# Optimization experiments

Hardware: AMD Instinct MI355X
Metric: run time of the kernel (lower is better)

The kernel has to match this reference:

```python
import jax, jax.numpy as jnp
import numpy as np

N = 8_388_608        # cohort size (2^23)
T_MAX = 1_000_000    # distinct time values -> ~8 ties per unique time


def setup_inputs() -> dict:
    key = jax.random.key(0)
    k1, k2, k3 = jax.random.split(key, 3)
    x = jax.random.normal(k1, (N,), dtype=jnp.float32)  # risk scores
    times = jax.random.randint(k2, (N,), 0, T_MAX).astype(jnp.float32)
    events = (jax.random.uniform(k3, (N,)) < 0.7).astype(jnp.float32)
    target = jnp.stack([times, events], axis=1)  # [N, 2] = [time, event]
    return {"input": x, "target": target}


def _cox_breslow_sqrt_loss(x, target):
    times = target[:, 0]
    events_all = target[:, 1]
    n = x.shape[0]
    # Sort by descending time (risk set = prefix in this ordering).
    sort_idx = jnp.argsort(-times)
    t = times[sort_idx]
    ev = events_all[sort_idx]
    xs = x[sort_idx]
    # Stable prefix log-sum-exp over the risk set.
    log_cum = jax.lax.cumlogsumexp(xs)
    # end_idx[i] = last index of the tie group containing i (groups are
    # contiguous after sorting). Reverse running-min over positions of
    # group-last elements.
    is_last = jnp.concatenate([t[:-1] != t[1:], jnp.ones((1,), dtype=bool)])
    pos = jnp.where(is_last, jnp.arange(n), n)
    end_idx = jnp.flip(jax.lax.cummin(jnp.flip(pos)))
    # Breslow: -sum(x*ev) + sum_groups logcum[group_end] * (#events in group)
    #        == -sum((x - logcum[end_idx]) * ev)
    loss = -jnp.sum((xs - log_cum[end_idx]) * ev)
    # reduction='mean' -> sqrt(loss / n)
    return jnp.sqrt(loss / n)


def reference(input, target):
    return _cox_breslow_sqrt_loss(input, target)
```

## Files before the change

kernel.cpp:

```cpp
#include <hip/hip_runtime.h>
#include <math.h>

#define TMAX 1000000
#define BINW 4096
#define BINSHIFT 12
#define NBIN 245
#define PADN (NBIN * BINW)
#define TILE 8192
#define NTHR 512
#define CAP 36864
#define CURSOR_STRIDE 16
#define BT_STRIDE 8
#define FIXSCALE 65536.0f
#define INV_FIXSCALE (1.0 / 65536.0)

#define OFF_SCAL     0
#define OFF_DONE     16
#define OFF_CURSOR   64
#define OFF_BINTOT   15744
#define OFF_PAYLOAD  31488
#define MEMSET_BYTES 31424
#define NEED_FULL    ((size_t)OFF_PAYLOAD + (size_t)NBIN * CAP * 4)
#define FB_BINTOT    15744
#define FB_CEXCL     17792
#define FB_BEXP      31488
#define FB_BEV       (FB_BEXP + PADN * 4)
#define NEED_MIN     ((size_t)FB_BEV + PADN * 4)

__device__ __forceinline__ int clamp_tau(float t) {
    int tau = (int)t;
    if (tau < 0) tau = 0;
    if (tau >= TMAX) tau = TMAX - 1;
    return tau;
}

__device__ __forceinline__ unsigned enc_payload(float xv, float tv, float ev_f, int* bin_out) {
    int tau = clamp_tau(tv);
    *bin_out = tau >> BINSHIFT;
    int fine = tau & (BINW - 1);
    float ex = __expf(xv);
    unsigned bb = __float_as_uint(ex);
    bb = (bb + 0x7FFFu + ((bb >> 16) & 1u)) >> 16;
    unsigned ev = (ev_f != 0.0f) ? 1u : 0u;
    return (bb << 16) | ((unsigned)fine << 1) | ev;
}

__device__ __forceinline__ float dec_exp(unsigned p) {
    return __uint_as_float((p >> 16) << 16);
}

__device__ __forceinline__ void hist1(unsigned long long* hist, unsigned p) {
    float ex = dec_exp(p);
    unsigned fx = __float2uint_rn(ex * FIXSCALE);
    unsigned long long add = ((unsigned long long)(p & 1u) << 48) | (unsigned long long)fx;
    atomicAdd(&hist[(p >> 1) & (BINW - 1)], add);
}

__device__ __forceinline__ void hist4(unsigned long long* hist, uint4 pv) {
    hist1(hist, pv.x); hist1(hist, pv.y); hist1(hist, pv.z); hist1(hist, pv.w);
}

__global__ __launch_bounds__(NTHR) void k_scatter(const float* __restrict__ x,
                                                  const float* __restrict__ tgt,
                                                  unsigned* __restrict__ cursor,
                                                  unsigned* __restrict__ payload,
                                                  double* __restrict__ bintot,
                                                  double* __restrict__ evx_out, int n) {
    __shared__ unsigned cnt[256];
    __shared__ unsigned lpre[256];
    __shared__ unsigned pay_lds[TILE];
    __shared__ unsigned char binof2[TILE / 2];
    __shared__ unsigned wtot_s[8];
    __shared__ double wpart[8];
    const int t = threadIdx.x;
    const int lane = t & 63;
    const int wv = t >> 6;
    if (t < 256) cnt[t] = 0;
    __syncthreads();

    const int tile0 = blockIdx.x * TILE;
    const int tilecount = min(TILE, n - tile0);
    unsigned pay[16], meta[16];
    double evx = 0.0;

    if (tilecount == TILE) {
        const float4* x4 = (const float4*)x;
        const float4* t4 = (const float4*)tgt;
        const int g0 = blockIdx.x * (TILE / 4);
#pragma unroll
        for (int j = 0; j < 4; ++j) {
            const int g = g0 + j * NTHR + t;
            float4 xv = x4[g];
            float4 ta = t4[2 * g];
            float4 tb = t4[2 * g + 1];
            float xs[4] = {xv.x, xv.y, xv.z, xv.w};
            float ts[4] = {ta.x, ta.z, tb.x, tb.z};
            float es[4] = {ta.y, ta.w, tb.y, tb.w};
#pragma unroll
            for (int e = 0; e < 4; ++e) {
                int bin;
                unsigned p = enc_payload(xs[e], ts[e], es[e], &bin);
                unsigned r = atomicAdd(&cnt[bin], 1u);
                pay[4 * j + e] = p;
                meta[4 * j + e] = ((unsigned)bin << 13) | r;
                if (p & 1) evx += (double)xs[e];
            }
        }
    } else {
        const float2* tg2 = (const float2*)tgt;
#pragma unroll
        for (int j = 0; j < 16; ++j) {
            int idx = tile0 + j * NTHR + t;
            if (idx < n) {
                float xv = x[idx];
                float2 te = tg2[idx];
                int bin;
                unsigned p = enc_payload(xv, te.x, te.y, &bin);
                unsigned r = atomicAdd(&cnt[bin], 1u);
                pay[j] = p;
                meta[j] = ((unsigned)bin << 13) | r;
                if (p & 1) evx += (double)xv;
            } else {
                meta[j] = 0xFFFFFFFFu;
            }
        }
    }
    __syncthreads();

    const unsigned c = (t < 256) ? cnt[t] : 0u;
    unsigned pfx = c;
#pragma unroll
    for (int d = 1; d < 64; d <<= 1) {
        unsigned u = __shfl_up(pfx, d);
        if (lane >= d) pfx += u;
    }
    if (lane == 63) wtot_s[wv] = pfx;
    __syncthreads();
    unsigned wbase = 0;
    if (t < 256) {
        for (int w = 0; w < wv; ++w) wbase += wtot_s[w];
    }
    const unsigned excl = (t < 256) ? (wbase + pfx - c) : 0u;
    if (t < 256) lpre[t] = excl;

    if (t < NBIN && c) cnt[t] = atomicAdd(&cursor[t * CURSOR_STRIDE], c);

    if (t < NBIN && c) {
        for (unsigned j = (excl + 1) >> 1; 2 * j < excl + c; ++j)
            binof2[j] = (unsigned char)t;
    }
    __syncthreads();

#pragma unroll
    for (int j = 0; j < 16; ++j) {
        if (meta[j] != 0xFFFFFFFFu) {
            unsigned bin = meta[j] >> 13;
            pay_lds[lpre[bin] + (meta[j] & 0x1FFFu)] = pay[j];
        }
    }
    __syncthreads();

    if (t < NBIN && c) {
        float s = 0.0f;
        for (unsigned k = excl; k < excl + c; ++k) s += dec_exp(pay_lds[k]);
        unsafeAtomicAdd(&bintot[t * BT_STRIDE], (double)s);
    }

    for (int k = t; k < tilecount; k += NTHR) {
        unsigned b = binof2[(unsigned)k >> 1];
        if (t & 1) {
            while ((unsigned)k >= lpre[b + 1]) ++b;
        }
        unsigned pos = cnt[b] + ((unsigned)k - lpre[b]);
        if (pos < CAP) payload[(size_t)b * CAP + pos] = pay_lds[k];
    }

#pragma unroll
    for (int d = 32; d > 0; d >>= 1) {
        double u = __shfl_down(evx, d);
        if (lane + d < 64) evx += u;
    }
    if (lane == 0) wpart[wv] = evx;
    __syncthreads();
    if (t == 0) {
        double s = 0.0;
        for (int w = 0; w < 8; ++w) s += wpart[w];
        atomicAdd(evx_out, s);
    }
}

__global__ __launch_bounds__(1024) void k_fused(const unsigned* __restrict__ payload,
                                                const unsigned* __restrict__ cursor,
                                                const double* __restrict__ bintot,
                                                double* __restrict__ scal,
                                                unsigned* __restrict__ done,
                                                float* __restrict__ out, int n) {
    __shared__ unsigned long long hist[BINW];
    __shared__ double wsumA[16];
    __shared__ double wsum[16];
    __shared__ double bcast;
    const int b = blockIdx.x;
    const int t = threadIdx.x;
    const int lane = t & 63;
    const int wv = t >> 6;

#pragma unroll
    for (int j = 0; j < BINW / 1024; ++j) hist[t + j * 1024] = 0ull;
    __syncthreads();

    unsigned cnt = cursor[b * CURSOR_STRIDE];
    if (cnt > CAP) cnt = CAP;
    const unsigned* seg = payload + (size_t)b * CAP;
    const uint4* seg4 = (const uint4*)seg;
    const unsigned n4 = cnt >> 2;
    unsigned i = t;
    for (; i + 1024 < n4; i += 2048) {
        uint4 a = seg4[i];
        uint4 c4 = seg4[i + 1024];
        hist4(hist, a);
        hist4(hist, c4);
    }
    for (; i < n4; i += 1024) hist4(hist, seg4[i]);
    for (unsigned k = (n4 << 2) + t; k < cnt; k += 1024) hist1(hist, seg[k]);
    __syncthreads();

    double ce = 0.0;
    for (int idx = b + 1 + t; idx < NBIN; idx += 1024) ce += bintot[idx * BT_STRIDE];
#pragma unroll
    for (int d = 32; d > 0; d >>= 1) {
        double u = __shfl_down(ce, d);
        if (lane + d < 64) ce += u;
    }
    if (lane == 0) wsumA[wv] = ce;
    __syncthreads();
    if (t == 0) {
        double s = 0.0;
        for (int w = 0; w < 16; ++w) s += wsumA[w];
        bcast = s;
    }
    __syncthreads();
    const double cexcl = bcast;

    const int tb = t * 4;
    double vex[4];
    unsigned vcnt[4];
    double segtot = 0.0;
#pragma unroll
    for (int j = 0; j < 4; ++j) {
        unsigned long long h = hist[tb + j];
        vex[j] = (double)(h & 0xFFFFFFFFFFFFull) * INV_FIXSCALE;
        vcnt[j] = (unsigned)(h >> 48);
        segtot += vex[j];
    }
    double isuf = segtot;
#pragma unroll
    for (int d = 1; d < 64; d <<= 1) {
        double u = __shfl_down(isuf, d);
        if (lane + d < 64) isuf += u;
    }
    if (lane == 0) wsum[wv] = isuf;
    __syncthreads();
    double wexcl = 0.0;
    for (int w = wv + 1; w < 16; ++w) wexcl += wsum[w];

    double run = cexcl + wexcl + (isuf - segtot);
    double local = 0.0;
#pragma unroll
    for (int j = 3; j >= 0; --j) {
        run += vex[j];
        if (vcnt[j]) local += (double)vcnt[j] * log(run);
    }

#pragma unroll
    for (int d = 32; d > 0; d >>= 1) {
        double u = __shfl_down(local, d);
        if (lane + d < 64) local += u;
    }
    if (lane == 0) wsumA[wv] = local;
    __syncthreads();
    if (t == 0) {
        double s = 0.0;
        for (int w = 0; w < 16; ++w) s += wsumA[w];
        unsafeAtomicAdd(&scal[1], s);
        __threadfence();
        unsigned tk = atomicAdd(done, 1u);
        if (tk == NBIN - 1) {
            double ld = unsafeAtomicAdd(&scal[1], 0.0);
            double loss = ld - scal[0];
            if (loss < 0.0) loss = 0.0;
            out[0] = (float)sqrt(loss / (double)n);
        }
    }
}

__global__ void k_accum(const float* __restrict__ x, const float* __restrict__ tgt,
                        float* __restrict__ bexp, float* __restrict__ bev,
                        double* __restrict__ evx_out, int ngroups) {
    double local = 0.0;
    const int nt = gridDim.x * blockDim.x;
    const int tid = blockIdx.x * blockDim.x + threadIdx.x;
    const float4* x4 = (const float4*)x;
    const float4* t4 = (const float4*)tgt;
    for (int g = tid; g < ngroups; g += nt) {
        float4 xv = x4[g];
        float4 ta = t4[2 * g];
        float4 tb = t4[2 * g + 1];
        float xs[4] = {xv.x, xv.y, xv.z, xv.w};
        float ts[4] = {ta.x, ta.z, tb.x, tb.z};
        float es[4] = {ta.y, ta.w, tb.y, tb.w};
#pragma unroll
        for (int j = 0; j < 4; ++j) {
            int tau = clamp_tau(ts[j]);
            unsafeAtomicAdd(&bexp[tau], __expf(xs[j]));
            if (es[j] != 0.0f) unsafeAtomicAdd(&bev[tau], es[j]);
            local += (double)(es[j] * xs[j]);
        }
    }
    __shared__ double sm[256];
    sm[threadIdx.x] = local;
    __syncthreads();
    for (int s = 128; s > 0; s >>= 1) {
        if (threadIdx.x < s) sm[threadIdx.x] += sm[threadIdx.x + s];
        __syncthreads();
    }
    if (threadIdx.x == 0) atomicAdd(evx_out, sm[0]);
}

__global__ void k_chunksum(const float* __restrict__ bexp, double* __restrict__ bintot) {
    const int b = blockIdx.x;
    double local = 0.0;
    for (int i = b * BINW + (int)threadIdx.x; i < (b + 1) * BINW; i += (int)blockDim.x)
        local += (double)bexp[i];
    __shared__ double sm[256];
    sm[threadIdx.x] = local;
    __syncthreads();
    for (int s = 128; s > 0; s >>= 1) {
        if (threadIdx.x < s) sm[threadIdx.x] += sm[threadIdx.x + s];
        __syncthreads();
    }
    if (threadIdx.x == 0) bintot[b] = sm[0];
}

__global__ __launch_bounds__(256) void k_scanbins(const double* __restrict__ bintot,
                                                  double* __restrict__ cexcl) {
    __shared__ double sm[256];
    const int t = threadIdx.x;
    sm[t] = (t < NBIN) ? bintot[t] : 0.0;
    __syncthreads();
    for (int d = 1; d < 256; d <<= 1) {
        double v = (t + d < 256) ? sm[t + d] : 0.0;
        __syncthreads();
        sm[t] += v;
        __syncthreads();
    }
    double e = (t + 1 < 256) ? sm[t + 1] : 0.0;
    __syncthreads();
    cexcl[t] = e;
}

__global__ __launch_bounds__(256) void k_logdot_g(const float* __restrict__ bexp,
                                                  const float* __restrict__ bev,
                                                  const double* __restrict__ cexcl,
                                                  double* __restrict__ logdot) {
    const int b = blockIdx.x;
    const int t = threadIdx.x;
    const float4* e4 = (const float4*)(bexp + b * BINW + t * 16);
    const float4* v4 = (const float4*)(bev + b * BINW + t * 16);
    float ve[16], vv[16];
#pragma unroll
    for (int q = 0; q < 4; ++q) {
        float4 a = e4[q], bb = v4[q];
        ve[4 * q] = a.x; ve[4 * q + 1] = a.y; ve[4 * q + 2] = a.z; ve[4 * q + 3] = a.w;
        vv[4 * q] = bb.x; vv[4 * q + 1] = bb.y; vv[4 * q + 2] = bb.z; vv[4 * q + 3] = bb.w;
    }
    double segtot = 0.0;
#pragma unroll
    for (int j = 0; j < 16; ++j) segtot += (double)ve[j];
    __shared__ double sm[256];
    sm[t] = segtot;
    __syncthreads();
    for (int d = 1; d < 256; d <<= 1) {
        double v = (t + d < 256) ? sm[t + d] : 0.0;
        __syncthreads();
        sm[t] += v;
        __syncthreads();
    }
    double excl = (t < 255) ? sm[t + 1] : 0.0;
    double run = cexcl[b] + excl;
    double local = 0.0;
#pragma unroll
    for (int j = 15; j >= 0; --j) {
        run += (double)ve[j];
        if (vv[j] > 0.0f) local += (double)vv[j] * log(run);
    }
    __syncthreads();
    sm[t] = local;
    __syncthreads();
    for (int s = 128; s > 0; s >>= 1) {
        if (t < s) sm[t] += sm[t + s];
        __syncthreads();
    }
    if (t == 0) atomicAdd(logdot, sm[0]);
}

__global__ void k_final(const double* __restrict__ scal, float* __restrict__ out, int n) {
    if (threadIdx.x == 0 && blockIdx.x == 0) {
        double loss = scal[1] - scal[0];
        if (loss < 0.0) loss = 0.0;
        out[0] = (float)sqrt(loss / (double)n);
    }
}

extern "C" void kernel_launch(void* const* d_in, const int* in_sizes, int n_in,
                              void* d_out, int out_size, void* d_ws, size_t ws_size,
                              hipStream_t stream) {
    const float* x = (const float*)d_in[0];
    const float* tgt = (const float*)d_in[1];
    float* out = (float*)d_out;
    int n = in_sizes[0];

    char* ws = (char*)d_ws;
    double* scal = (double*)(ws + OFF_SCAL);
    unsigned* done = (unsigned*)(ws + OFF_DONE);
    unsigned* cursor = (unsigned*)(ws + OFF_CURSOR);
    double* bintot = (double*)(ws + OFF_BINTOT);
    unsigned* payload = (unsigned*)(ws + OFF_PAYLOAD);

    if (ws_size >= NEED_FULL) {
        hipMemsetAsync(ws, 0, MEMSET_BYTES, stream);
        const int nblk = (n + TILE - 1) / TILE;
        k_scatter<<<nblk, NTHR, 0, stream>>>(x, tgt, cursor, payload, bintot, scal, n);
        k_fused<<<NBIN, 1024, 0, stream>>>(payload, cursor, bintot, scal, done, out, n);
    } else if (ws_size >= NEED_MIN) {
        float* bexp = (float*)(ws + FB_BEXP);
        float* bev = (float*)(ws + FB_BEV);
        double* bintotF = (double*)(ws + FB_BINTOT);
        double* cexclF = (double*)(ws + FB_CEXCL);
        hipMemsetAsync(ws, 0, NEED_MIN, stream);
        k_accum<<<2048, 256, 0, stream>>>(x, tgt, bexp, bev, scal, n / 4);
        k_chunksum<<<NBIN, 256, 0, stream>>>(bexp, bintotF);
        k_scanbins<<<1, 256, 0, stream>>>(bintotF, cexclF);
        k_logdot_g<<<NBIN, 256, 0, stream>>>(bexp, bev, cexclF, scal + 1);
        k_final<<<1, 1, 0, stream>>>(scal, out, n);
    }
}
```

Measured before the change: 163.3 us.

## Fuse memset, scatter and bin-histogram passes into one cooperative persistent kernel

Replaces the memset, scatter kernel and fused per-bin kernel with a single cooperative kernel that zeroes the workspace, scatters tiles in a grid-stride loop, grid-syncs, then runs the per-bin histogram and log-sum pass. This removes two launch boundaries and the separate memset. In exchange it adds grid-wide barriers and a persistent grid sized from occupancy, capped at 1024 blocks. The per-bin phase now uses 512 threads instead of 1024, and the old path is kept as a fallback if the cooperative launch fails.

```diff
diff --git a/kernel.cpp b/kernel.cpp
--- a/kernel.cpp
+++ b/kernel.cpp
@@ -1,5 +1,8 @@
 #include <hip/hip_runtime.h>
+#include <hip/hip_cooperative_groups.h>
 #include <math.h>
+
+namespace cg = cooperative_groups;
 
 #define TMAX 1000000
 #define BINW 4096
@@ -27,6 +30,8 @@
 #define FB_BEV       (FB_BEXP + PADN * 4)
 #define NEED_MIN     ((size_t)FB_BEV + PADN * 4)
 
+#define SMEM_BYTES 39008
+
 __device__ __forceinline__ int clamp_tau(float t) {
     int tau = (int)t;
     if (tau < 0) tau = 0;
@@ -58,6 +63,254 @@
 
 __device__ __forceinline__ void hist4(unsigned long long* hist, uint4 pv) {
     hist1(hist, pv.x); hist1(hist, pv.y); hist1(hist, pv.z); hist1(hist, pv.w);
+}
+
+__global__ __launch_bounds__(NTHR, 8) void k_all(const float* __restrict__ x,
+                                                 const float* __restrict__ tgt,
+                                                 char* __restrict__ ws,
+                                                 float* __restrict__ out,
+                                                 int n, int ntiles) {
+    __shared__ __align__(16) unsigned char smem[SMEM_BYTES];
+
+    unsigned* cursor = (unsigned*)(ws + OFF_CURSOR);
+    double* bintot = (double*)(ws + OFF_BINTOT);
+    unsigned* payload = (unsigned*)(ws + OFF_PAYLOAD);
+    double* scal = (double*)(ws + OFF_SCAL);
+    unsigned* done = (unsigned*)(ws + OFF_DONE);
+
+    const int t = threadIdx.x;
+    const int lane = t & 63;
+    const int wv = t >> 6;
+
+    cg::grid_group grid = cg::this_grid();
+
+    {
+        unsigned* wsw = (unsigned*)ws;
+        for (unsigned w = blockIdx.x * NTHR + (unsigned)t; w < MEMSET_BYTES / 4;
+             w += gridDim.x * NTHR)
+            wsw[w] = 0u;
+    }
+    __threadfence();
+    grid.sync();
+
+    unsigned* pay_lds = (unsigned*)smem;
+    unsigned char* binof2 = (unsigned char*)(smem + 32768);
+    unsigned* cnt = (unsigned*)(smem + 36864);
+    unsigned* lpre = (unsigned*)(smem + 37888);
+    unsigned* wtot_s = (unsigned*)(smem + 38912);
+    double* wpart = (double*)(smem + 38944);
+
+    double evx = 0.0;
+    for (int tile = blockIdx.x; tile < ntiles; tile += gridDim.x) {
+        __syncthreads();
+        if (t < 256) cnt[t] = 0;
+        __syncthreads();
+
+        const int tile0 = tile * TILE;
+        const int tilecount = min(TILE, n - tile0);
+        unsigned pay[16], meta[16];
+
+        if (tilecount == TILE) {
+            const float4* x4 = (const float4*)x;
+            const float4* t4 = (const float4*)tgt;
+            const int g0 = tile * (TILE / 4);
+#pragma unroll
+            for (int j = 0; j < 4; ++j) {
+                const int g = g0 + j * NTHR + t;
+                float4 xv = x4[g];
+                float4 ta = t4[2 * g];
+                float4 tb = t4[2 * g + 1];
+                float xs[4] = {xv.x, xv.y, xv.z, xv.w};
+                float ts[4] = {ta.x, ta.z, tb.x, tb.z};
+                float es[4] = {ta.y, ta.w, tb.y, tb.w};
+#pragma unroll
+                for (int e = 0; e < 4; ++e) {
+                    int bin;
+                    unsigned p = enc_payload(xs[e], ts[e], es[e], &bin);
+                    unsigned r = atomicAdd(&cnt[bin], 1u);
+                    pay[4 * j + e] = p;
+                    meta[4 * j + e] = ((unsigned)bin << 13) | r;
+                    if (p & 1) evx += (double)xs[e];
+                }
+            }
+        } else {
+            const float2* tg2 = (const float2*)tgt;
+#pragma unroll
+            for (int j = 0; j < 16; ++j) {
+                int idx = tile0 + j * NTHR + t;
+                if (idx < n) {
+                    float xv = x[idx];
+                    float2 te = tg2[idx];
+                    int bin;
+                    unsigned p = enc_payload(xv, te.x, te.y, &bin);
+                    unsigned r = atomicAdd(&cnt[bin], 1u);
+                    pay[j] = p;
+                    meta[j] = ((unsigned)bin << 13) | r;
+                    if (p & 1) evx += (double)xv;
+                } else {
+                    meta[j] = 0xFFFFFFFFu;
+                }
+            }
+        }
+        __syncthreads();
+
+        const unsigned c = (t < 256) ? cnt[t] : 0u;
+        unsigned pfx = c;
+#pragma unroll
+        for (int d = 1; d < 64; d <<= 1) {
+            unsigned u = __shfl_up(pfx, d);
+            if (lane >= d) pfx += u;
+        }
+        if (lane == 63) wtot_s[wv] = pfx;
+        __syncthreads();
+        unsigned wbase = 0;
+        if (t < 256) {
+            for (int w = 0; w < wv; ++w) wbase += wtot_s[w];
+        }
+        const unsigned excl = (t < 256) ? (wbase + pfx - c) : 0u;
+        if (t < 256) lpre[t] = excl;
+
+        if (t < NBIN && c) cnt[t] = atomicAdd(&cursor[t * CURSOR_STRIDE], c);
+
+        if (t < NBIN && c) {
+            for (unsigned j = (excl + 1) >> 1; 2 * j < excl + c; ++j)
+                binof2[j] = (unsigned char)t;
+        }
+        __syncthreads();
+
+#pragma unroll
+        for (int j = 0; j < 16; ++j) {
+            if (meta[j] != 0xFFFFFFFFu) {
+                unsigned bin = meta[j] >> 13;
+                pay_lds[lpre[bin] + (meta[j] & 0x1FFFu)] = pay[j];
+            }
+        }
+        __syncthreads();
+
+        if (t < NBIN && c) {
+            float s = 0.0f;
+            for (unsigned k = excl; k < excl + c; ++k) s += dec_exp(pay_lds[k]);
+            unsafeAtomicAdd(&bintot[t * BT_STRIDE], (double)s);
+        }
+
+        for (int k = t; k < tilecount; k += NTHR) {
+            unsigned b = binof2[(unsigned)k >> 1];
+            if (t & 1) {
+                while ((unsigned)k >= lpre[b + 1]) ++b;
+            }
+            unsigned pos = cnt[b] + ((unsigned)k - lpre[b]);
+            if (pos < CAP) payload[(size_t)b * CAP + pos] = pay_lds[k];
+        }
+    }
+
+#pragma unroll
+    for (int d = 32; d > 0; d >>= 1) {
+        double u = __shfl_down(evx, d);
+        if (lane + d < 64) evx += u;
+    }
+    if (lane == 0) wpart[wv] = evx;
+    __syncthreads();
+    if (t == 0) {
+        double s = 0.0;
+        for (int w = 0; w < 8; ++w) s += wpart[w];
+        atomicAdd(&scal[0], s);
+    }
+
+    __threadfence();
+    grid.sync();
+
+    unsigned long long* hist = (unsigned long long*)smem;
+    double* wsumA = (double*)(smem + 32768);
+    double* wsum = (double*)(smem + 32832);
+    double* bcastp = (double*)(smem + 32896);
+
+    for (int b = blockIdx.x; b < NBIN; b += gridDim.x) {
+        __syncthreads();
+#pragma unroll
+        for (int j = 0; j < BINW / NTHR; ++j) hist[t + j * NTHR] = 0ull;
+        __syncthreads();
+
+        unsigned cntb = cursor[b * CURSOR_STRIDE];
+        if (cntb > CAP) cntb = CAP;
+        const unsigned* seg = payload + (size_t)b * CAP;
+        const uint4* seg4 = (const uint4*)seg;
+        const unsigned n4 = cntb >> 2;
+        unsigned i = t;
+        for (; i + NTHR < n4; i += 2 * NTHR) {
+            uint4 a = seg4[i];
+            uint4 c4 = seg4[i + NTHR];
+            hist4(hist, a);
+            hist4(hist, c4);
+        }
+        for (; i < n4; i += NTHR) hist4(hist, seg4[i]);
+        for (unsigned k = (n4 << 2) + t; k < cntb; k += NTHR) hist1(hist, seg[k]);
+        __syncthreads();
+
+        double ce = 0.0;
+        for (int idx = b + 1 + t; idx < NBIN; idx += NTHR) ce += bintot[idx * BT_STRIDE];
+#pragma unroll
+        for (int d = 32; d > 0; d >>= 1) {
+            double u = __shfl_down(ce, d);
+            if (lane + d < 64) ce += u;
+        }
+        if (lane == 0) wsumA[wv] = ce;
+        __syncthreads();
+        if (t == 0) {
+            double s = 0.0;
+            for (int w = 0; w < 8; ++w) s += wsumA[w];
+            *bcastp = s;
+        }
+        __syncthreads();
+        const double cexcl = *bcastp;
+
+        const int tb = t * (BINW / NTHR);
+        double segtot = 0.0;
+#pragma unroll
+        for (int j = 0; j < BINW / NTHR; ++j)
+            segtot += (double)(hist[tb + j] & 0xFFFFFFFFFFFFull) * INV_FIXSCALE;
+        double isuf = segtot;
+#pragma unroll
+        for (int d = 1; d < 64; d <<= 1) {
+            double u = __shfl_down(isuf, d);
+            if (lane + d < 64) isuf += u;
+        }
+        if (lane == 0) wsum[wv] = isuf;
+        __syncthreads();
+        double wexcl = 0.0;
+        for (int w = wv + 1; w < 8; ++w) wexcl += wsum[w];
+
+        double run = cexcl + wexcl + (isuf - segtot);
+        double local = 0.0;
+#pragma unroll
+        for (int j = BINW / NTHR - 1; j >= 0; --j) {
+            unsigned long long h = hist[tb + j];
+            double v = (double)(h & 0xFFFFFFFFFFFFull) * INV_FIXSCALE;
+            unsigned cc = (unsigned)(h >> 48);
+            run += v;
+            if (cc) local += (double)cc * log(run);
+        }
+
+#pragma unroll
+        for (int d = 32; d > 0; d >>= 1) {
+            double u = __shfl_down(local, d);
+            if (lane + d < 64) local += u;
+        }
+        if (lane == 0) wsumA[wv] = local;
+        __syncthreads();
+        if (t == 0) {
+            double s = 0.0;
+            for (int w = 0; w < 8; ++w) s += wsumA[w];
+            unsafeAtomicAdd(&scal[1], s);
+            __threadfence();
+            unsigned tk = atomicAdd(done, 1u);
+            if (tk == NBIN - 1) {
+                double ld = unsafeAtomicAdd(&scal[1], 0.0);
+                double loss = ld - scal[0];
+                if (loss < 0.0) loss = 0.0;
+                out[0] = (float)sqrt(loss / (double)n);
+            }
+        }
+    }
 }
 
 __global__ __launch_bounds__(NTHR) void k_scatter(const float* __restrict__ x,
@@ -418,20 +671,48 @@
     const float* tgt = (const float*)d_in[1];
     float* out = (float*)d_out;
     int n = in_sizes[0];
-
     char* ws = (char*)d_ws;
-    double* scal = (double*)(ws + OFF_SCAL);
-    unsigned* done = (unsigned*)(ws + OFF_DONE);
-    unsigned* cursor = (unsigned*)(ws + OFF_CURSOR);
-    double* bintot = (double*)(ws + OFF_BINTOT);
-    unsigned* payload = (unsigned*)(ws + OFF_PAYLOAD);
 
     if (ws_size >= NEED_FULL) {
-        hipMemsetAsync(ws, 0, MEMSET_BYTES, stream);
-        const int nblk = (n + TILE - 1) / TILE;
-        k_scatter<<<nblk, NTHR, 0, stream>>>(x, tgt, cursor, payload, bintot, scal, n);
-        k_fused<<<NBIN, 1024, 0, stream>>>(payload, cursor, bintot, scal, done, out, n);
+        static int coop_grid = 0;
+        if (coop_grid == 0) {
+            int dev = 0;
+            (void)hipGetDevice(&dev);
+            int cus = 0;
+            if (hipDeviceGetAttribute(&cus, hipDeviceAttributeMultiprocessorCount, dev) !=
+                    hipSuccess || cus <= 0)
+                cus = 256;
+            int nb = 0;
+            if (hipOccupancyMaxActiveBlocksPerMultiprocessor(&nb, k_all, NTHR, 0) !=
+                    hipSuccess || nb < 1)
+                nb = 1;
+            long g = (long)nb * (long)cus;
+            if (g > 1024) g = 1024;
+            if (g < 1) g = 1;
+            coop_grid = (int)g;
+        }
+        int ntiles = (n + TILE - 1) / TILE;
+        const float* xa = x;
+        const float* ta = tgt;
+        char* wsa = ws;
+        float* oa = out;
+        int na = n, nta = ntiles;
+        void* args[] = {(void*)&xa, (void*)&ta, (void*)&wsa, (void*)&oa, (void*)&na, (void*)&nta};
+        hipError_t err = hipLaunchCooperativeKernel(k_all, dim3(coop_grid), dim3(NTHR),
+                                                    args, 0, stream);
+        if (err != hipSuccess) {
+            double* scal = (double*)(ws + OFF_SCAL);
+            unsigned* done = (unsigned*)(ws + OFF_DONE);
+            unsigned* cursor = (unsigned*)(ws + OFF_CURSOR);
+            double* bintot = (double*)(ws + OFF_BINTOT);
+            unsigned* payload = (unsigned*)(ws + OFF_PAYLOAD);
+            hipMemsetAsync(ws, 0, MEMSET_BYTES, stream);
+            const int nblk = (n + TILE - 1) / TILE;
+            k_scatter<<<nblk, NTHR, 0, stream>>>(x, tgt, cursor, payload, bintot, scal, n);
+            k_fused<<<NBIN, 1024, 0, stream>>>(payload, cursor, bintot, scal, done, out, n);
+        }
     } else if (ws_size >= NEED_MIN) {
+        double* scal = (double*)(ws + OFF_SCAL);
         float* bexp = (float*)(ws + FB_BEXP);
         float* bev = (float*)(ws + FB_BEV);
         double* bintotF = (double*)(ws + FB_BINTOT);
```

Result: slower. 425.6 us (+160.7%).
